# Kernel optimization log

Hardware: AMD Instinct MI355X
Metric: run time of the kernel (lower is better)

## Reference

```python
import jax, jax.numpy as jnp
import numpy as np

H, HKV, HD = 16, 4, 128
EPS = 1.1920928955078125e-07  # float32 eps, torch F.rms_norm default


def _rms_norm(t):
    return t * jax.lax.rsqrt(jnp.mean(t * t, axis=-1, keepdims=True) + EPS)


def _rope(t, cos, sin):
    # t: [B, T, h, HD]; cos/sin: [T, HD//2] -> broadcast [1, T, 1, HD//2]
    te, to = t[..., 0::2], t[..., 1::2]
    c = cos[None, :, None, :]
    s = sin[None, :, None, :]
    re = te * c - to * s
    ro = te * s + to * c
    return jnp.stack((re, ro), axis=-1).reshape(t.shape)


def setup_inputs() -> dict:
    key = jax.random.key(0)
    ks = jax.random.split(key, 5)
    B, T, C = 2, 2048, 2048
    return {
        "x": jax.random.normal(ks[0], (B, T, C), jnp.float32),
        "Wq": jax.random.normal(ks[1], (C, C), jnp.float32) * 0.02,
        "Wk": jax.random.normal(ks[2], (HKV * HD, C), jnp.float32) * 0.02,
        "Wv": jax.random.normal(ks[3], (HKV * HD, C), jnp.float32) * 0.02,
        "Wo": jax.random.normal(ks[4], (C, C), jnp.float32) * 0.02,
        "q_gain": jnp.full((H,), 5.0, jnp.float32),
    }


def reference(x, Wq, Wk, Wv, Wo, q_gain):
    B, T, C = x.shape
    q = (x @ Wq.T).reshape(B, T, H, HD)
    k = (x @ Wk.T).reshape(B, T, HKV, HD)
    v = (x @ Wv.T).reshape(B, T, HKV, HD)

    q = _rms_norm(q)
    k = _rms_norm(k)

    theta = 1.0 / (10000.0 ** (jnp.arange(0, HD, 2, dtype=jnp.float32) / HD))
    t = jnp.arange(T, dtype=jnp.float32)
    freqs = jnp.outer(t, theta)  # [T, HD//2]
    cos, sin = jnp.cos(freqs), jnp.sin(freqs)

    q = _rope(q, cos, sin)
    k = _rope(k, cos, sin)
    q = q * q_gain[None, None, :, None]

    qh = q.transpose(0, 2, 1, 3)                       # [B, H, T, HD]
    kh = jnp.repeat(k.transpose(0, 2, 1, 3), H // HKV, axis=1)
    vh = jnp.repeat(v.transpose(0, 2, 1, 3), H // HKV, axis=1)

    scale = 1.0 / jnp.sqrt(jnp.float32(HD))
    scores = jnp.einsum("bhqd,bhkd->bhqk", qh, kh) * scale
    causal = jnp.tril(jnp.ones((T, T), bool))
    scores = jnp.where(causal[None, None], scores, jnp.finfo(scores.dtype).min)
    attn = jax.nn.softmax(scores, axis=-1)
    out = jnp.einsum("bhqk,bhkd->bhqd", attn, vh)
    out = out.transpose(0, 2, 1, 3).reshape(B, T, C)
    return out @ Wo.T
```

## Files before the change

kernel.cpp:

```cpp
#include <hip/hip_runtime.h>
#include <hip/hip_bf16.h>

#define TSEQ 2048
#define CDIM 2048
#define NH   16
#define NKV  4
#define HDIM 128
#define BATCH 2
#define MROWS (BATCH*TSEQ)
#define KVC   (NKV*HDIM)
#define QKVC  (CDIM + 2*KVC)

typedef short bf16x8 __attribute__((ext_vector_type(8)));
typedef float f32x4  __attribute__((ext_vector_type(4)));

typedef const __attribute__((address_space(1))) void* gptr_t;
typedef __attribute__((address_space(3))) void* sptr_t;

__device__ inline void async16(const __hip_bfloat16* g, __hip_bfloat16* l) {
  __builtin_amdgcn_global_load_lds((gptr_t)g, (sptr_t)l, 16, 0, 0);
}

__device__ inline f32x4 mfma16(bf16x8 a, bf16x8 b, f32x4 c) {
  return __builtin_amdgcn_mfma_f32_16x16x32_bf16(a, b, c, 0, 0, 0);
}

__device__ inline float bfbits2f(unsigned short u) {
  return __uint_as_float(((unsigned)u) << 16);
}

__device__ inline unsigned short f2bfu(float x) {
  __hip_bfloat16 t = __float2bfloat16(x);
  return *(unsigned short*)&t;
}

__device__ inline int swz128(int row, int col) {
  return row*128 + (((col >> 3) ^ (row & 15)) << 3) + (col & 7);
}
__device__ inline int swz64(int row, int col) {
  return row*64 + ((((col >> 3) ^ row) & 7) << 3) + (col & 7);
}

__global__ void canary(const void* __restrict__ x, int* __restrict__ flag) {
  __shared__ int cnt[256];
  int tid = threadIdx.x;
  const unsigned short* u = (const unsigned short*)x;
  int c = 0;
#pragma unroll
  for (int i = 0; i < 4; ++i) {
    float a = fabsf(bfbits2f(u[(tid*4 + i)*2]));
    if (a >= 1e-6f && a <= 1e3f) c++;
  }
  cnt[tid] = c;
  __syncthreads();
  for (int s = 128; s > 0; s >>= 1) {
    if (tid < s) cnt[tid] += cnt[tid + s];
    __syncthreads();
  }
  if (tid == 0) *flag = (cnt[0] > 512) ? 1 : 0;
}

__global__ __launch_bounds__(256) void canonize_all(
    const void* __restrict__ xs,  const void* __restrict__ wqs,
    const void* __restrict__ wks, const void* __restrict__ wvs,
    const void* __restrict__ wos, const void* __restrict__ gs,
    __hip_bfloat16* __restrict__ xd,
    __hip_bfloat16* __restrict__ wqkv,
    __hip_bfloat16* __restrict__ wod,
    __hip_bfloat16* __restrict__ gd,
    const int* __restrict__ flag)
{
  int blk = blockIdx.x;
  const void* src; __hip_bfloat16* dst; int base, n;
  if      (blk < 4096) { src = xs;  dst = xd;                base = blk;        n = MROWS*CDIM; }
  else if (blk < 6144) { src = wqs; dst = wqkv;              base = blk - 4096; n = CDIM*CDIM; }
  else if (blk < 6656) { src = wks; dst = wqkv + (size_t)CDIM*CDIM;            base = blk - 6144; n = KVC*CDIM; }
  else if (blk < 7168) { src = wvs; dst = wqkv + (size_t)(CDIM+KVC)*CDIM;      base = blk - 6656; n = KVC*CDIM; }
  else if (blk < 9216) { src = wos; dst = wod;               base = blk - 7168; n = CDIM*CDIM; }
  else                 { src = gs;  dst = gd;                base = 0;          n = NH; }
  int idx = base*2048 + threadIdx.x*8;
  if (idx >= n) return;
  if (*flag) {
    *(bf16x8*)&dst[idx] = *(const bf16x8*)((const __hip_bfloat16*)src + idx);
  } else {
    const float* s = (const float*)src + idx;
#pragma unroll
    for (int j = 0; j < 8; ++j) dst[idx + j] = __float2bfloat16(s[j]);
  }
}

#define BK 64

__global__ __launch_bounds__(512, 2) void gemm_bt256(
    const __hip_bfloat16* __restrict__ A,
    const __hip_bfloat16* __restrict__ B,
    __hip_bfloat16* __restrict__ C,
    int M, int N, int K, int lda)
{
  __shared__ __align__(16) __hip_bfloat16 As[2][256*BK];
  __shared__ __align__(16) __hip_bfloat16 Bs[2][256*BK];
  const int tid  = threadIdx.x;
  const int wave = tid >> 6;
  const int lane = tid & 63;
  const int qd   = lane >> 4;
  const int ln   = lane & 15;
  const int m0   = blockIdx.y * 256;
  const int n0   = blockIdx.x * 256;
  const int wm   = (wave >> 2) * 128;
  const int wn   = (wave & 3) * 64;

  auto stageA = [&](int half, int buf, int kt) {
    const __hip_bfloat16* src = A + (size_t)(m0 + half*128)*lda + kt*BK;
    __hip_bfloat16* dst = &As[buf][half*128*BK];
#pragma unroll
    for (int i = 0; i < 2; ++i) {
      int c = i*512 + tid;
      int row = c >> 3, sl = c & 7;
      int gs = sl ^ (row & 7);
      async16(&src[(size_t)row*lda + gs*8], &dst[(i*512 + wave*64)*8]);
    }
  };
  auto stageB = [&](int half, int buf, int kt) {
    const __hip_bfloat16* src = B + (size_t)(n0 + half*128)*K + kt*BK;
    __hip_bfloat16* dst = &Bs[buf][half*128*BK];
#pragma unroll
    for (int i = 0; i < 2; ++i) {
      int c = i*512 + tid;
      int row = c >> 3, sl = c & 7;
      int gs = sl ^ (row & 7);
      async16(&src[(size_t)row*K + gs*8], &dst[(i*512 + wave*64)*8]);
    }
  };
  auto ldA = [&](int buf, int m, int kk) -> bf16x8 {
    int row = wm + m*16 + ln;
    return *(const bf16x8*)&As[buf][row*BK + (((kk*4 + qd) ^ (row & 7)) << 3)];
  };
  auto ldB = [&](int buf, int n, int kk) -> bf16x8 {
    int row = wn + n*16 + ln;
    return *(const bf16x8*)&Bs[buf][row*BK + (((kk*4 + qd) ^ (row & 7)) << 3)];
  };

  f32x4 acc[8][4] = {};
  const int nt = K / BK;

  stageA(0, 0, 0); stageA(1, 0, 0);
  stageB(0, 0, 0); stageB(1, 0, 0);
  if (nt > 1) {
    stageA(0, 1, 1); stageA(1, 1, 1);
    asm volatile("s_waitcnt vmcnt(4)" ::: "memory");
  } else {
    asm volatile("s_waitcnt vmcnt(0)" ::: "memory");
  }
  __builtin_amdgcn_s_barrier();

#pragma unroll 1
  for (int t = 0; t < nt; ++t) {
    const int buf = t & 1;
    bf16x8 a03[4][2], a47[4][2], b01[2][2], b23[2][2];

#pragma unroll
    for (int m = 0; m < 4; ++m)
#pragma unroll
      for (int kk = 0; kk < 2; ++kk) a03[m][kk] = ldA(buf, m, kk);
#pragma unroll
    for (int n = 0; n < 2; ++n)
#pragma unroll
      for (int kk = 0; kk < 2; ++kk) b01[n][kk] = ldB(buf, n, kk);
    if (t + 1 < nt) { stageB(0, buf ^ 1, t + 1); stageB(1, buf ^ 1, t + 1); }
    __builtin_amdgcn_s_setprio(1);
#pragma unroll
    for (int m = 0; m < 4; ++m)
#pragma unroll
      for (int n = 0; n < 2; ++n)
#pragma unroll
        for (int kk = 0; kk < 2; ++kk)
          acc[m][n] = mfma16(a03[m][kk], b01[n][kk], acc[m][n]);
    __builtin_amdgcn_s_setprio(0);
    __builtin_amdgcn_s_barrier();

#pragma unroll
    for (int m = 0; m < 4; ++m)
#pragma unroll
      for (int kk = 0; kk < 2; ++kk) a47[m][kk] = ldA(buf, 4 + m, kk);
    __builtin_amdgcn_s_setprio(1);
#pragma unroll
    for (int m = 0; m < 4; ++m)
#pragma unroll
      for (int n = 0; n < 2; ++n)
#pragma unroll
        for (int kk = 0; kk < 2; ++kk)
          acc[4 + m][n] = mfma16(a47[m][kk], b01[n][kk], acc[4 + m][n]);
    __builtin_amdgcn_s_setprio(0);
    __builtin_amdgcn_s_barrier();

#pragma unroll
    for (int n = 0; n < 2; ++n)
#pragma unroll
      for (int kk = 0; kk < 2; ++kk) b23[n][kk] = ldB(buf, 2 + n, kk);
    __builtin_amdgcn_s_setprio(1);
#pragma unroll
    for (int m = 0; m < 4; ++m)
#pragma unroll
      for (int n = 0; n < 2; ++n)
#pragma unroll
        for (int kk = 0; kk < 2; ++kk)
          acc[m][2 + n] = mfma16(a03[m][kk], b23[n][kk], acc[m][2 + n]);
    __builtin_amdgcn_s_setprio(0);
    __builtin_amdgcn_s_barrier();

    if (t + 2 < nt) { stageA(0, buf, t + 2); stageA(1, buf, t + 2); }
    __builtin_amdgcn_s_setprio(1);
#pragma unroll
    for (int m = 0; m < 4; ++m)
#pragma unroll
      for (int n = 0; n < 2; ++n)
#pragma unroll
        for (int kk = 0; kk < 2; ++kk)
          acc[4 + m][2 + n] = mfma16(a47[m][kk], b23[n][kk], acc[4 + m][2 + n]);
    __builtin_amdgcn_s_setprio(0);
    if (t + 2 < nt) asm volatile("s_waitcnt vmcnt(4)" ::: "memory");
    else            asm volatile("s_waitcnt vmcnt(0)" ::: "memory");
    __builtin_amdgcn_s_barrier();
  }

#pragma unroll
  for (int m = 0; m < 8; ++m)
#pragma unroll
    for (int n = 0; n < 4; ++n) {
      int row = m0 + wm + m*16 + qd*4;
      int col = n0 + wn + n*16 + ln;
#pragma unroll
      for (int r = 0; r < 4; ++r)
        C[(size_t)(row + r)*N + col] = __float2bfloat16(acc[m][n][r]);
    }
}

__global__ __launch_bounds__(256, 2) void gemm_out(
    const __hip_bfloat16* __restrict__ A,
    const __hip_bfloat16* __restrict__ B,
    void* __restrict__ C,
    int M, int N, int K, int lda, const int* __restrict__ flag)
{
  __shared__ __align__(16) __hip_bfloat16 As[128*32];
  __shared__ __align__(16) __hip_bfloat16 Bs[128*32];
  const int tid  = threadIdx.x;
  const int wave = tid >> 6;
  const int lane = tid & 63;
  const int qd   = lane >> 4;
  const int ln   = lane & 15;
  const int m0   = blockIdx.y * 128;
  const int n0   = blockIdx.x * 128;
  const int wm   = (wave >> 1) * 64;
  const int wn   = (wave & 1) * 64;

  f32x4 acc[4][4] = {};

  for (int k0 = 0; k0 < K; k0 += 32) {
    __syncthreads();
#pragma unroll
    for (int r = 0; r < 2; ++r) {
      int e   = (r*256 + tid) * 8;
      int row = e >> 5;
      int col = e & 31;
      async16(&A[(size_t)(m0+row)*lda + k0 + col], &As[(size_t)(r*256 + wave*64)*8]);
      async16(&B[(size_t)(n0+row)*K   + k0 + col], &Bs[(size_t)(r*256 + wave*64)*8]);
    }
    __syncthreads();
    bf16x8 af[4], bfr[4];
#pragma unroll
    for (int i = 0; i < 4; ++i)
      af[i] = *(const bf16x8*)&As[(wm + i*16 + ln)*32 + qd*8];
#pragma unroll
    for (int j = 0; j < 4; ++j)
      bfr[j] = *(const bf16x8*)&Bs[(wn + j*16 + ln)*32 + qd*8];
#pragma unroll
    for (int i = 0; i < 4; ++i)
#pragma unroll
      for (int j = 0; j < 4; ++j)
        acc[i][j] = mfma16(af[i], bfr[j], acc[i][j]);
  }
  const bool isbf = (*flag != 0);
#pragma unroll
  for (int i = 0; i < 4; ++i)
#pragma unroll
    for (int j = 0; j < 4; ++j) {
      int row = m0 + wm + i*16 + qd*4;
      int col = n0 + wn + j*16 + ln;
#pragma unroll
      for (int r = 0; r < 4; ++r) {
        if (isbf) ((__hip_bfloat16*)C)[(size_t)(row + r)*N + col] = __float2bfloat16(acc[i][j][r]);
        else      ((float*)C)[(size_t)(row + r)*N + col] = acc[i][j][r];
      }
    }
}

__global__ __launch_bounds__(256) void prep_qk(
    __hip_bfloat16* __restrict__ qkv,
    const __hip_bfloat16* __restrict__ gain)
{
  int wid  = blockIdx.x * 4 + (threadIdx.x >> 6);
  int lane = threadIdx.x & 63;
  bool isq = wid < MROWS*NH;
  int m, h;
  __hip_bfloat16* p;
  if (isq) { m = wid >> 4; h = wid & 15; p = qkv + (size_t)m*QKVC + h*HDIM; }
  else     { int w2 = wid - MROWS*NH; m = w2 >> 2; h = w2 & 3; p = qkv + (size_t)m*QKVC + CDIM + h*HDIM; }

  ushort2 raw = *(const ushort2*)((const unsigned short*)p + 2*lane);
  float e = bfbits2f(raw.x), o = bfbits2f(raw.y);
  float ss = e*e + o*o;
#pragma unroll
  for (int off = 32; off >= 1; off >>= 1) ss += __shfl_xor(ss, off);
  float rms = rsqrtf(ss * (1.0f/128.0f) + 1.1920928955078125e-07f);
  e *= rms; o *= rms;

  float theta = exp2f(-(float)(2*lane) * (1.0f/128.0f) * 13.287712379549449f);
  int t = m & (TSEQ-1);
  float fr = (float)t * theta;
  float c = cosf(fr), s = sinf(fr);
  float re = e*c - o*s;
  float ro = e*s + o*c;

  if (isq) {
    float g = bfbits2f(*(const unsigned short*)&gain[h]) * 0.08838834764831845f;
    re *= g; ro *= g;
  }
  p[2*lane]   = __float2bfloat16(re);
  p[2*lane+1] = __float2bfloat16(ro);
}

__global__ __launch_bounds__(256) void transpose_v(
    const __hip_bfloat16* __restrict__ qkv, __hip_bfloat16* __restrict__ vt)
{
  __shared__ __hip_bfloat16 tile[32][34];
  int tx = threadIdx.x & 31;
  int ty = threadIdx.x >> 5;
  int r0 = blockIdx.x * 32;
  int c0 = blockIdx.y * 32;
#pragma unroll
  for (int i = 0; i < 4; ++i)
    tile[ty + i*8][tx] = qkv[(size_t)(r0 + ty + i*8)*QKVC + (CDIM + KVC) + c0 + tx];
  __syncthreads();
  int b = r0 >> 11;
  int t = r0 & (TSEQ-1);
  int hk = c0 >> 7;
  int d0 = c0 & (HDIM-1);
#pragma unroll
  for (int i = 0; i < 4; ++i) {
    int d = d0 + ty + i*8;
    vt[((size_t)((b*NKV + hk)*HDIM + d))*TSEQ + t + tx] = tile[tx][ty + i*8];
  }
}

__global__ __launch_bounds__(256, 2) void attn_kernel(
    const __hip_bfloat16* __restrict__ qkv,
    const __hip_bfloat16* __restrict__ vt,
    __hip_bfloat16* __restrict__ out)
{
  const int tid  = threadIdx.x;
  const int wave = tid >> 6;
  const int lane = tid & 63;
  const int qd = lane >> 4, ln = lane & 15;
  const int p  = blockIdx.x;
  const int h  = blockIdx.y;
  const int b  = blockIdx.z;
  const int hk = h >> 2;

  const __hip_bfloat16* K = qkv + (size_t)(b*TSEQ)*QKVC + CDIM + hk*HDIM;
  const __hip_bfloat16* V = vt + ((size_t)(b*NKV + hk)*HDIM)*TSEQ;

  __shared__ __align__(16) __hip_bfloat16 Ks[64*128];
  __shared__ __align__(16) __hip_bfloat16 Vs[128*64];
  __shared__ __align__(16) __hip_bfloat16 Pb[64*64];
  __shared__ float Lb[4][64];

  auto issueK = [&](int t0) {
#pragma unroll
    for (int i = 0; i < 4; ++i) {
      int c = i*256 + tid;
      int row = c >> 4, cc = c & 15;
      int gcc = cc ^ (row & 15);
      async16(&K[(size_t)(t0 + row)*QKVC + gcc*8], &Ks[(i*256 + wave*64)*8]);
    }
  };
  auto issueV = [&](int t0) {
#pragma unroll
    for (int i = 0; i < 4; ++i) {
      int c = i*256 + tid;
      int row = c >> 3, cc = c & 7;
      int gcc = cc ^ (row & 7);
      async16(&V[(size_t)row*TSEQ + t0 + gcc*8], &Vs[(i*256 + wave*64)*8]);
    }
  };

#pragma unroll 1
  for (int seg = 0; seg < 2; ++seg) {
    const int qt = seg ? (31 - p) : p;
    const int q0 = qt * 64;

    bf16x8 qfr[4][4];
#pragma unroll
    for (int qsub = 0; qsub < 4; ++qsub)
#pragma unroll
      for (int kc = 0; kc < 4; ++kc)
        qfr[qsub][kc] = *(const bf16x8*)&qkv[((size_t)(b*TSEQ + q0 + qsub*16 + ln))*QKVC + h*HDIM + kc*32 + qd*8];

    f32x4 o[2][4] = {};
    float lacc[4] = {0.f, 0.f, 0.f, 0.f};

    __syncthreads();
    issueK(0);
    __syncthreads();

#pragma unroll 1
    for (int kt = 0; kt <= qt; ++kt) {
      const int t0 = kt * 64;
      issueV(t0);

      f32x4 sc[4] = {};
#pragma unroll
      for (int kc = 0; kc < 4; ++kc) {
        bf16x8 kfa = *(const bf16x8*)&Ks[swz128(wave*16 + ln, kc*32 + qd*8)];
#pragma unroll
        for (int qsub = 0; qsub < 4; ++qsub)
          sc[qsub] = mfma16(kfa, qfr[qsub][kc], sc[qsub]);
      }
      if (kt == qt) {
#pragma unroll
        for (int qsub = 0; qsub < 4; ++qsub)
#pragma unroll
          for (int r = 0; r < 4; ++r) {
            int kv = t0 + wave*16 + qd*4 + r;
            int q  = q0 + qsub*16 + ln;
            if (kv > q) sc[qsub][r] = -1.0e30f;
          }
      }
#pragma unroll
      for (int qsub = 0; qsub < 4; ++qsub) {
#pragma unroll
        for (int r = 0; r < 4; ++r)
          sc[qsub][r] = __expf(sc[qsub][r]);
        lacc[qsub] += (sc[qsub][0] + sc[qsub][1]) + (sc[qsub][2] + sc[qsub][3]);
      }

#pragma unroll
      for (int qsub = 0; qsub < 4; ++qsub) {
        ushort4 pk;
        pk.x = f2bfu(sc[qsub][0]); pk.y = f2bfu(sc[qsub][1]);
        pk.z = f2bfu(sc[qsub][2]); pk.w = f2bfu(sc[qsub][3]);
        *(ushort4*)&Pb[swz64(qsub*16 + ln, wave*16 + qd*4)] = pk;
      }

      __syncthreads();
      if (kt < qt) issueK(t0 + 64);

      __builtin_amdgcn_s_setprio(1);
#pragma unroll
      for (int kc2 = 0; kc2 < 2; ++kc2) {
        bf16x8 pfb[4];
#pragma unroll
        for (int qsub = 0; qsub < 4; ++qsub)
          pfb[qsub] = *(const bf16x8*)&Pb[swz64(qsub*16 + ln, kc2*32 + qd*8)];
#pragma unroll
        for (int half = 0; half < 2; ++half) {
          bf16x8 vfa = *(const bf16x8*)&Vs[swz64(wave*32 + half*16 + ln, kc2*32 + qd*8)];
#pragma unroll
          for (int qsub = 0; qsub < 4; ++qsub)
            o[half][qsub] = mfma16(vfa, pfb[qsub], o[half][qsub]);
        }
      }
      __builtin_amdgcn_s_setprio(0);
      __syncthreads();
    }

#pragma unroll
    for (int qsub = 0; qsub < 4; ++qsub) {
      lacc[qsub] += __shfl_xor(lacc[qsub], 16);
      lacc[qsub] += __shfl_xor(lacc[qsub], 32);
    }
    if (qd == 0) {
#pragma unroll
      for (int qsub = 0; qsub < 4; ++qsub)
        Lb[wave][qsub*16 + ln] = lacc[qsub];
    }
    __syncthreads();
    float inv[4];
#pragma unroll
    for (int qsub = 0; qsub < 4; ++qsub) {
      int q = qsub*16 + ln;
      inv[qsub] = 1.0f / (((Lb[0][q] + Lb[1][q]) + (Lb[2][q] + Lb[3][q])));
    }

#pragma unroll
    for (int half = 0; half < 2; ++half)
#pragma unroll
      for (int qsub = 0; qsub < 4; ++qsub) {
        ushort4 pk;
        pk.x = f2bfu(o[half][qsub][0] * inv[qsub]);
        pk.y = f2bfu(o[half][qsub][1] * inv[qsub]);
        pk.z = f2bfu(o[half][qsub][2] * inv[qsub]);
        pk.w = f2bfu(o[half][qsub][3] * inv[qsub]);
        *(ushort4*)&Ks[swz128(qsub*16 + ln, wave*32 + half*16 + qd*4)] = pk;
      }
    __syncthreads();
#pragma unroll
    for (int pass = 0; pass < 4; ++pass) {
      int row = wave*16 + pass*4 + qd;
      bf16x8 val = *(const bf16x8*)&Ks[swz128(row, ln*8)];
      int q = q0 + row;
      *(bf16x8*)&out[((size_t)(b*TSEQ + q))*CDIM + h*HDIM + ln*8] = val;
    }
  }
}

extern "C" void kernel_launch(void* const* d_in, const int* in_sizes, int n_in,
                              void* d_out, int out_size, void* d_ws, size_t ws_size,
                              hipStream_t stream) {
  char* ws = (char*)d_ws;
  size_t off = 0;
  auto alloc = [&](size_t bytes) { char* p = ws + off; off += (bytes + 255) & ~(size_t)255; return p; };

  int* flag = (int*)alloc(256);
  __hip_bfloat16* xb   = (__hip_bfloat16*)alloc((size_t)MROWS*CDIM*2);
  __hip_bfloat16* wqkv = (__hip_bfloat16*)alloc((size_t)QKVC*CDIM*2);
  __hip_bfloat16* wob  = (__hip_bfloat16*)alloc((size_t)CDIM*CDIM*2);
  __hip_bfloat16* gb   = (__hip_bfloat16*)alloc(256);
  __hip_bfloat16* qkv  = (__hip_bfloat16*)alloc((size_t)MROWS*QKVC*2);
  __hip_bfloat16* vt   = (__hip_bfloat16*)alloc((size_t)MROWS*KVC*2);

  canary<<<1, 256, 0, stream>>>(d_in[0], flag);

  canonize_all<<<9217, 256, 0, stream>>>(
      d_in[0], d_in[1], d_in[2], d_in[3], d_in[4], d_in[5],
      xb, wqkv, wob, gb, flag);

  gemm_bt256<<<dim3(QKVC/256, MROWS/256), 512, 0, stream>>>(
      xb, wqkv, qkv, MROWS, QKVC, CDIM, CDIM);

  int nwaves = MROWS*NH + MROWS*NKV;
  prep_qk<<<nwaves/4, 256, 0, stream>>>(qkv, gb);

  transpose_v<<<dim3(MROWS/32, KVC/32), 256, 0, stream>>>(qkv, vt);

  attn_kernel<<<dim3(16, NH, BATCH), 256, 0, stream>>>(qkv, vt, xb);

  gemm_out<<<dim3(CDIM/128, MROWS/128), 256, 0, stream>>>(
      xb, wob, d_out, MROWS, CDIM, CDIM, CDIM, flag);
}
```

Before: 294.5 us.

## Retile QKV GEMM to 256x192 and rebuild output GEMM with pipelined 128x256 tiles

The QKV projection GEMM moves from 256x256 to 256x192 tiles, so N=3072 splits into 16 column blocks and the grid grows to fill more CUs. The output projection GEMM drops its simple single-buffered 128x128 BK=32 kernel for a 512-thread, double-buffered, swizzled 128x256 BK=64 kernel with async LDS staging and interleaved MFMA phases. Both changes aim to raise MFMA utilisation and hide global-load latency. The cost is more LDS and registers per block, and possibly lower occupancy.

```diff
diff --git a/kernel.cpp b/kernel.cpp
--- a/kernel.cpp
+++ b/kernel.cpp
@@ -98,20 +98,157 @@
     int M, int N, int K, int lda)
 {
   __shared__ __align__(16) __hip_bfloat16 As[2][256*BK];
+  __shared__ __align__(16) __hip_bfloat16 Bs[2][192*BK];
+  const int tid  = threadIdx.x;
+  const int wave = tid >> 6;
+  const int lane = tid & 63;
+  const int qd   = lane >> 4;
+  const int ln   = lane & 15;
+  const int m0   = blockIdx.y * 256;
+  const int n0   = blockIdx.x * 192;
+  const int wm   = (wave >> 2) * 128;
+  const int wn   = (wave & 3) * 48;
+
+  auto stageA = [&](int buf, int kt) {
+    const __hip_bfloat16* src = A + (size_t)m0*lda + kt*BK;
+    __hip_bfloat16* dst = &As[buf][0];
+#pragma unroll
+    for (int i = 0; i < 4; ++i) {
+      int c = i*512 + tid;
+      int row = c >> 3, sl = c & 7;
+      int gs = sl ^ (row & 7);
+      async16(&src[(size_t)row*lda + gs*8], &dst[(i*512 + wave*64)*8]);
+    }
+  };
+  auto stageB = [&](int buf, int kt) {
+    const __hip_bfloat16* src = B + (size_t)n0*K + kt*BK;
+    __hip_bfloat16* dst = &Bs[buf][0];
+#pragma unroll
+    for (int i = 0; i < 3; ++i) {
+      int c = i*512 + tid;
+      int row = c >> 3, sl = c & 7;
+      int gs = sl ^ (row & 7);
+      async16(&src[(size_t)row*K + gs*8], &dst[(i*512 + wave*64)*8]);
+    }
+  };
+  auto ldA = [&](int buf, int m, int kk) -> bf16x8 {
+    int row = wm + m*16 + ln;
+    return *(const bf16x8*)&As[buf][row*BK + (((kk*4 + qd) ^ (row & 7)) << 3)];
+  };
+  auto ldB = [&](int buf, int n, int kk) -> bf16x8 {
+    int row = wn + n*16 + ln;
+    return *(const bf16x8*)&Bs[buf][row*BK + (((kk*4 + qd) ^ (row & 7)) << 3)];
+  };
+
+  f32x4 acc[8][3] = {};
+  const int nt = K / BK;
+
+  stageA(0, 0); stageB(0, 0);
+  if (nt > 1) {
+    stageA(1, 1); stageB(1, 1);
+    asm volatile("s_waitcnt vmcnt(7)" ::: "memory");
+  } else {
+    asm volatile("s_waitcnt vmcnt(0)" ::: "memory");
+  }
+  __builtin_amdgcn_s_barrier();
+
+#pragma unroll 1
+  for (int t = 0; t < nt; ++t) {
+    const int buf = t & 1;
+    bf16x8 a03[4][2], a47[4][2], b01[2][2], b2[2];
+
+#pragma unroll
+    for (int m = 0; m < 4; ++m)
+#pragma unroll
+      for (int kk = 0; kk < 2; ++kk) a03[m][kk] = ldA(buf, m, kk);
+#pragma unroll
+    for (int n = 0; n < 2; ++n)
+#pragma unroll
+      for (int kk = 0; kk < 2; ++kk) b01[n][kk] = ldB(buf, n, kk);
+    __builtin_amdgcn_s_setprio(1);
+#pragma unroll
+    for (int m = 0; m < 4; ++m)
+#pragma unroll
+      for (int n = 0; n < 2; ++n)
+#pragma unroll
+        for (int kk = 0; kk < 2; ++kk)
+          acc[m][n] = mfma16(a03[m][kk], b01[n][kk], acc[m][n]);
+    __builtin_amdgcn_s_setprio(0);
+    __builtin_amdgcn_s_barrier();
+
+#pragma unroll
+    for (int m = 0; m < 4; ++m)
+#pragma unroll
+      for (int kk = 0; kk < 2; ++kk) a47[m][kk] = ldA(buf, 4 + m, kk);
+    __builtin_amdgcn_s_setprio(1);
+#pragma unroll
+    for (int m = 0; m < 4; ++m)
+#pragma unroll
+      for (int n = 0; n < 2; ++n)
+#pragma unroll
+        for (int kk = 0; kk < 2; ++kk)
+          acc[4 + m][n] = mfma16(a47[m][kk], b01[n][kk], acc[4 + m][n]);
+    __builtin_amdgcn_s_setprio(0);
+    __builtin_amdgcn_s_barrier();
+
+#pragma unroll
+    for (int kk = 0; kk < 2; ++kk) b2[kk] = ldB(buf, 2, kk);
+    if (t + 2 < nt) stageA(buf, t + 2);
+    __builtin_amdgcn_s_setprio(1);
+#pragma unroll
+    for (int m = 0; m < 4; ++m)
+#pragma unroll
+      for (int kk = 0; kk < 2; ++kk)
+        acc[m][2] = mfma16(a03[m][kk], b2[kk], acc[m][2]);
+    __builtin_amdgcn_s_setprio(0);
+    __builtin_amdgcn_s_barrier();
+
+    if (t + 2 < nt) stageB(buf, t + 2);
+    __builtin_amdgcn_s_setprio(1);
+#pragma unroll
+    for (int m = 0; m < 4; ++m)
+#pragma unroll
+      for (int kk = 0; kk < 2; ++kk)
+        acc[4 + m][2] = mfma16(a47[m][kk], b2[kk], acc[4 + m][2]);
+    __builtin_amdgcn_s_setprio(0);
+    if (t + 2 < nt) asm volatile("s_waitcnt vmcnt(7)" ::: "memory");
+    else            asm volatile("s_waitcnt vmcnt(0)" ::: "memory");
+    __builtin_amdgcn_s_barrier();
+  }
+
+#pragma unroll
+  for (int m = 0; m < 8; ++m)
+#pragma unroll
+    for (int n = 0; n < 3; ++n) {
+      int row = m0 + wm + m*16 + qd*4;
+      int col = n0 + wn + n*16 + ln;
+#pragma unroll
+      for (int r = 0; r < 4; ++r)
+        C[(size_t)(row + r)*N + col] = __float2bfloat16(acc[m][n][r]);
+    }
+}
+
+__global__ __launch_bounds__(512, 2) void gemm_out(
+    const __hip_bfloat16* __restrict__ A,
+    const __hip_bfloat16* __restrict__ B,
+    void* __restrict__ C,
+    int M, int N, int K, int lda, const int* __restrict__ flag)
+{
+  __shared__ __align__(16) __hip_bfloat16 As[2][128*BK];
   __shared__ __align__(16) __hip_bfloat16 Bs[2][256*BK];
   const int tid  = threadIdx.x;
   const int wave = tid >> 6;
   const int lane = tid & 63;
   const int qd   = lane >> 4;
   const int ln   = lane & 15;
-  const int m0   = blockIdx.y * 256;
+  const int m0   = blockIdx.y * 128;
   const int n0   = blockIdx.x * 256;
-  const int wm   = (wave >> 2) * 128;
+  const int wm   = (wave >> 2) * 64;
   const int wn   = (wave & 3) * 64;
 
-  auto stageA = [&](int half, int buf, int kt) {
-    const __hip_bfloat16* src = A + (size_t)(m0 + half*128)*lda + kt*BK;
-    __hip_bfloat16* dst = &As[buf][half*128*BK];
+  auto stageA = [&](int buf, int kt) {
+    const __hip_bfloat16* src = A + (size_t)m0*lda + kt*BK;
+    __hip_bfloat16* dst = &As[buf][0];
 #pragma unroll
     for (int i = 0; i < 2; ++i) {
       int c = i*512 + tid;
@@ -120,11 +257,11 @@
       async16(&src[(size_t)row*lda + gs*8], &dst[(i*512 + wave*64)*8]);
     }
   };
-  auto stageB = [&](int half, int buf, int kt) {
-    const __hip_bfloat16* src = B + (size_t)(n0 + half*128)*K + kt*BK;
-    __hip_bfloat16* dst = &Bs[buf][half*128*BK];
-#pragma unroll
-    for (int i = 0; i < 2; ++i) {
+  auto stageB = [&](int buf, int kt) {
+    const __hip_bfloat16* src = B + (size_t)n0*K + kt*BK;
+    __hip_bfloat16* dst = &Bs[buf][0];
+#pragma unroll
+    for (int i = 0; i < 4; ++i) {
       int c = i*512 + tid;
       int row = c >> 3, sl = c & 7;
       int gs = sl ^ (row & 7);
@@ -140,14 +277,13 @@
     return *(const bf16x8*)&Bs[buf][row*BK + (((kk*4 + qd) ^ (row & 7)) << 3)];
   };
 
-  f32x4 acc[8][4] = {};
+  f32x4 acc[4][4] = {};
   const int nt = K / BK;
 
-  stageA(0, 0, 0); stageA(1, 0, 0);
-  stageB(0, 0, 0); stageB(1, 0, 0);
+  stageA(0, 0); stageB(0, 0);
   if (nt > 1) {
-    stageA(0, 1, 1); stageA(1, 1, 1);
-    asm volatile("s_waitcnt vmcnt(4)" ::: "memory");
+    stageA(1, 1); stageB(1, 1);
+    asm volatile("s_waitcnt vmcnt(6)" ::: "memory");
   } else {
     asm volatile("s_waitcnt vmcnt(0)" ::: "memory");
   }
@@ -156,40 +292,39 @@
 #pragma unroll 1
   for (int t = 0; t < nt; ++t) {
     const int buf = t & 1;
-    bf16x8 a03[4][2], a47[4][2], b01[2][2], b23[2][2];
-
-#pragma unroll
-    for (int m = 0; m < 4; ++m)
-#pragma unroll
-      for (int kk = 0; kk < 2; ++kk) a03[m][kk] = ldA(buf, m, kk);
+    bf16x8 a01[2][2], a23[2][2], b01[2][2], b23[2][2];
+
+#pragma unroll
+    for (int m = 0; m < 2; ++m)
+#pragma unroll
+      for (int kk = 0; kk < 2; ++kk) a01[m][kk] = ldA(buf, m, kk);
 #pragma unroll
     for (int n = 0; n < 2; ++n)
 #pragma unroll
       for (int kk = 0; kk < 2; ++kk) b01[n][kk] = ldB(buf, n, kk);
-    if (t + 1 < nt) { stageB(0, buf ^ 1, t + 1); stageB(1, buf ^ 1, t + 1); }
-    __builtin_amdgcn_s_setprio(1);
-#pragma unroll
-    for (int m = 0; m < 4; ++m)
+    __builtin_amdgcn_s_setprio(1);
+#pragma unroll
+    for (int m = 0; m < 2; ++m)
 #pragma unroll
       for (int n = 0; n < 2; ++n)
 #pragma unroll
         for (int kk = 0; kk < 2; ++kk)
-          acc[m][n] = mfma16(a03[m][kk], b01[n][kk], acc[m][n]);
-    __builtin_amdgcn_s_setprio(0);
-    __builtin_amdgcn_s_barrier();
-
-#pragma unroll
-    for (int m = 0; m < 4; ++m)
-#pragma unroll
-      for (int kk = 0; kk < 2; ++kk) a47[m][kk] = ldA(buf, 4 + m, kk);
-    __builtin_amdgcn_s_setprio(1);
-#pragma unroll
-    for (int m = 0; m < 4; ++m)
+          acc[m][n] = mfma16(a01[m][kk], b01[n][kk], acc[m][n]);
+    __builtin_amdgcn_s_setprio(0);
+    __builtin_amdgcn_s_barrier();
+
+#pragma unroll
+    for (int m = 0; m < 2; ++m)
+#pragma unroll
+      for (int kk = 0; kk < 2; ++kk) a23[m][kk] = ldA(buf, 2 + m, kk);
+    __builtin_amdgcn_s_setprio(1);
+#pragma unroll
+    for (int m = 0; m < 2; ++m)
 #pragma unroll
       for (int n = 0; n < 2; ++n)
 #pragma unroll
         for (int kk = 0; kk < 2; ++kk)
-          acc[4 + m][n] = mfma16(a47[m][kk], b01[n][kk], acc[4 + m][n]);
+          acc[2 + m][n] = mfma16(a23[m][kk], b01[n][kk], acc[2 + m][n]);
     __builtin_amdgcn_s_setprio(0);
     __builtin_amdgcn_s_barrier();
 
@@ -197,99 +332,44 @@
     for (int n = 0; n < 2; ++n)
 #pragma unroll
       for (int kk = 0; kk < 2; ++kk) b23[n][kk] = ldB(buf, 2 + n, kk);
-    __builtin_amdgcn_s_setprio(1);
-#pragma unroll
-    for (int m = 0; m < 4; ++m)
+    if (t + 2 < nt) stageA(buf, t + 2);
+    __builtin_amdgcn_s_setprio(1);
+#pragma unroll
+    for (int m = 0; m < 2; ++m)
 #pragma unroll
       for (int n = 0; n < 2; ++n)
 #pragma unroll
         for (int kk = 0; kk < 2; ++kk)
-          acc[m][2 + n] = mfma16(a03[m][kk], b23[n][kk], acc[m][2 + n]);
-    __builtin_amdgcn_s_setprio(0);
-    __builtin_amdgcn_s_barrier();
-
-    if (t + 2 < nt) { stageA(0, buf, t + 2); stageA(1, buf, t + 2); }
-    __builtin_amdgcn_s_setprio(1);
-#pragma unroll
-    for (int m = 0; m < 4; ++m)
+          acc[m][2 + n] = mfma16(a01[m][kk], b23[n][kk], acc[m][2 + n]);
+    __builtin_amdgcn_s_setprio(0);
+    __builtin_amdgcn_s_barrier();
+
+    if (t + 2 < nt) stageB(buf, t + 2);
+    __builtin_amdgcn_s_setprio(1);
+#pragma unroll
+    for (int m = 0; m < 2; ++m)
 #pragma unroll
       for (int n = 0; n < 2; ++n)
 #pragma unroll
         for (int kk = 0; kk < 2; ++kk)
-          acc[4 + m][2 + n] = mfma16(a47[m][kk], b23[n][kk], acc[4 + m][2 + n]);
-    __builtin_amdgcn_s_setprio(0);
-    if (t + 2 < nt) asm volatile("s_waitcnt vmcnt(4)" ::: "memory");
+          acc[2 + m][2 + n] = mfma16(a23[m][kk], b23[n][kk], acc[2 + m][2 + n]);
+    __builtin_amdgcn_s_setprio(0);
+    if (t + 2 < nt) asm volatile("s_waitcnt vmcnt(6)" ::: "memory");
     else            asm volatile("s_waitcnt vmcnt(0)" ::: "memory");
     __builtin_amdgcn_s_barrier();
   }
 
-#pragma unroll
-  for (int m = 0; m < 8; ++m)
+  const bool isbf = (*flag != 0);
+#pragma unroll
+  for (int m = 0; m < 4; ++m)
 #pragma unroll
     for (int n = 0; n < 4; ++n) {
       int row = m0 + wm + m*16 + qd*4;
       int col = n0 + wn + n*16 + ln;
 #pragma unroll
-      for (int r = 0; r < 4; ++r)
-        C[(size_t)(row + r)*N + col] = __float2bfloat16(acc[m][n][r]);
-    }
-}
-
-__global__ __launch_bounds__(256, 2) void gemm_out(
-    const __hip_bfloat16* __restrict__ A,
-    const __hip_bfloat16* __restrict__ B,
-    void* __restrict__ C,
-    int M, int N, int K, int lda, const int* __restrict__ flag)
-{
-  __shared__ __align__(16) __hip_bfloat16 As[128*32];
-  __shared__ __align__(16) __hip_bfloat16 Bs[128*32];
-  const int tid  = threadIdx.x;
-  const int wave = tid >> 6;
-  const int lane = tid & 63;
-  const int qd   = lane >> 4;
-  const int ln   = lane & 15;
-  const int m0   = blockIdx.y * 128;
-  const int n0   = blockIdx.x * 128;
-  const int wm   = (wave >> 1) * 64;
-  const int wn   = (wave & 1) * 64;
-
-  f32x4 acc[4][4] = {};
-
-  for (int k0 = 0; k0 < K; k0 += 32) {
-    __syncthreads();
-#pragma unroll
-    for (int r = 0; r < 2; ++r) {
-      int e   = (r*256 + tid) * 8;
-      int row = e >> 5;
-      int col = e & 31;
-      async16(&A[(size_t)(m0+row)*lda + k0 + col], &As[(size_t)(r*256 + wave*64)*8]);
-      async16(&B[(size_t)(n0+row)*K   + k0 + col], &Bs[(size_t)(r*256 + wave*64)*8]);
-    }
-    __syncthreads();
-    bf16x8 af[4], bfr[4];
-#pragma unroll
-    for (int i = 0; i < 4; ++i)
-      af[i] = *(const bf16x8*)&As[(wm + i*16 + ln)*32 + qd*8];
-#pragma unroll
-    for (int j = 0; j < 4; ++j)
-      bfr[j] = *(const bf16x8*)&Bs[(wn + j*16 + ln)*32 + qd*8];
-#pragma unroll
-    for (int i = 0; i < 4; ++i)
-#pragma unroll
-      for (int j = 0; j < 4; ++j)
-        acc[i][j] = mfma16(af[i], bfr[j], acc[i][j]);
-  }
-  const bool isbf = (*flag != 0);
-#pragma unroll
-  for (int i = 0; i < 4; ++i)
-#pragma unroll
-    for (int j = 0; j < 4; ++j) {
-      int row = m0 + wm + i*16 + qd*4;
-      int col = n0 + wn + j*16 + ln;
-#pragma unroll
       for (int r = 0; r < 4; ++r) {
-        if (isbf) ((__hip_bfloat16*)C)[(size_t)(row + r)*N + col] = __float2bfloat16(acc[i][j][r]);
-        else      ((float*)C)[(size_t)(row + r)*N + col] = acc[i][j][r];
+        if (isbf) ((__hip_bfloat16*)C)[(size_t)(row + r)*N + col] = __float2bfloat16(acc[m][n][r]);
+        else      ((float*)C)[(size_t)(row + r)*N + col] = acc[m][n][r];
       }
     }
 }
@@ -534,7 +614,7 @@
       d_in[0], d_in[1], d_in[2], d_in[3], d_in[4], d_in[5],
       xb, wqkv, wob, gb, flag);
 
-  gemm_bt256<<<dim3(QKVC/256, MROWS/256), 512, 0, stream>>>(
+  gemm_bt256<<<dim3(QKVC/192, MROWS/256), 512, 0, stream>>>(
       xb, wqkv, qkv, MROWS, QKVC, CDIM, CDIM);
 
   int nwaves = MROWS*NH + MROWS*NKV;
@@ -544,6 +624,6 @@
 
   attn_kernel<<<dim3(16, NH, BATCH), 256, 0, stream>>>(qkv, vt, xb);
 
-  gemm_out<<<dim3(CDIM/128, MROWS/128), 256, 0, stream>>>(
+  gemm_out<<<dim3(CDIM/256, MROWS/128), 512, 0, stream>>>(
       xb, wob, d_out, MROWS, CDIM, CDIM, CDIM, flag);
 }
```

New measurement: 295.8 us. Within noise of the previous version (+0.5%).

## Retile QKV GEMM to 256x192 tiles, vectorize canonize and prep_qk

Applied to the files above, without the earlier changes.

Changes the fused QKV projection GEMM tile from 256x256 to 256x192. QKVC=3072 then divides into 16 column tiles, for 256 blocks total against the CU count. The staging schedule changes so A and B for tile t+2 are prefetched mid-iteration, with vmcnt thresholds adjusted to match. The fp32->bf16 canonize path now uses float4 loads and a single 16-byte store. prep_qk handles two head-rows per wave with 4-element vector loads and stores. The retiling trades per-block MFMA reuse for better CU balance, and the reordered prefetch schedule risks subtle pipeline hazards.

```diff
diff --git a/kernel.cpp b/kernel.cpp
--- a/kernel.cpp
+++ b/kernel.cpp
@@ -84,8 +84,14 @@
     *(bf16x8*)&dst[idx] = *(const bf16x8*)((const __hip_bfloat16*)src + idx);
   } else {
     const float* s = (const float*)src + idx;
-#pragma unroll
-    for (int j = 0; j < 8; ++j) dst[idx + j] = __float2bfloat16(s[j]);
+    float4 f0 = *(const float4*)s;
+    float4 f1 = *(const float4*)(s + 4);
+    union { bf16x8 v; unsigned short u[8]; } o;
+    o.u[0] = f2bfu(f0.x); o.u[1] = f2bfu(f0.y);
+    o.u[2] = f2bfu(f0.z); o.u[3] = f2bfu(f0.w);
+    o.u[4] = f2bfu(f1.x); o.u[5] = f2bfu(f1.y);
+    o.u[6] = f2bfu(f1.z); o.u[7] = f2bfu(f1.w);
+    *(bf16x8*)&dst[idx] = o.v;
   }
 }
 
@@ -98,33 +104,33 @@
     int M, int N, int K, int lda)
 {
   __shared__ __align__(16) __hip_bfloat16 As[2][256*BK];
-  __shared__ __align__(16) __hip_bfloat16 Bs[2][256*BK];
+  __shared__ __align__(16) __hip_bfloat16 Bs[2][192*BK];
   const int tid  = threadIdx.x;
   const int wave = tid >> 6;
   const int lane = tid & 63;
   const int qd   = lane >> 4;
   const int ln   = lane & 15;
   const int m0   = blockIdx.y * 256;
-  const int n0   = blockIdx.x * 256;
+  const int n0   = blockIdx.x * 192;
   const int wm   = (wave >> 2) * 128;
-  const int wn   = (wave & 3) * 64;
-
-  auto stageA = [&](int half, int buf, int kt) {
-    const __hip_bfloat16* src = A + (size_t)(m0 + half*128)*lda + kt*BK;
-    __hip_bfloat16* dst = &As[buf][half*128*BK];
-#pragma unroll
-    for (int i = 0; i < 2; ++i) {
+  const int wn   = (wave & 3) * 48;
+
+  auto stageA = [&](int buf, int kt) {
+    const __hip_bfloat16* src = A + (size_t)m0*lda + kt*BK;
+    __hip_bfloat16* dst = &As[buf][0];
+#pragma unroll
+    for (int i = 0; i < 4; ++i) {
       int c = i*512 + tid;
       int row = c >> 3, sl = c & 7;
       int gs = sl ^ (row & 7);
       async16(&src[(size_t)row*lda + gs*8], &dst[(i*512 + wave*64)*8]);
     }
   };
-  auto stageB = [&](int half, int buf, int kt) {
-    const __hip_bfloat16* src = B + (size_t)(n0 + half*128)*K + kt*BK;
-    __hip_bfloat16* dst = &Bs[buf][half*128*BK];
-#pragma unroll
-    for (int i = 0; i < 2; ++i) {
+  auto stageB = [&](int buf, int kt) {
+    const __hip_bfloat16* src = B + (size_t)n0*K + kt*BK;
+    __hip_bfloat16* dst = &Bs[buf][0];
+#pragma unroll
+    for (int i = 0; i < 3; ++i) {
       int c = i*512 + tid;
       int row = c >> 3, sl = c & 7;
       int gs = sl ^ (row & 7);
@@ -140,14 +146,13 @@
     return *(const bf16x8*)&Bs[buf][row*BK + (((kk*4 + qd) ^ (row & 7)) << 3)];
   };
 
-  f32x4 acc[8][4] = {};
+  f32x4 acc[8][3] = {};
   const int nt = K / BK;
 
-  stageA(0, 0, 0); stageA(1, 0, 0);
-  stageB(0, 0, 0); stageB(1, 0, 0);
+  stageA(0, 0); stageB(0, 0);
   if (nt > 1) {
-    stageA(0, 1, 1); stageA(1, 1, 1);
-    asm volatile("s_waitcnt vmcnt(4)" ::: "memory");
+    stageA(1, 1); stageB(1, 1);
+    asm volatile("s_waitcnt vmcnt(7)" ::: "memory");
   } else {
     asm volatile("s_waitcnt vmcnt(0)" ::: "memory");
   }
@@ -156,7 +161,7 @@
 #pragma unroll 1
   for (int t = 0; t < nt; ++t) {
     const int buf = t & 1;
-    bf16x8 a03[4][2], a47[4][2], b01[2][2], b23[2][2];
+    bf16x8 a03[4][2], a47[4][2], b01[2][2], b2[2];
 
 #pragma unroll
     for (int m = 0; m < 4; ++m)
@@ -166,7 +171,6 @@
     for (int n = 0; n < 2; ++n)
 #pragma unroll
       for (int kk = 0; kk < 2; ++kk) b01[n][kk] = ldB(buf, n, kk);
-    if (t + 1 < nt) { stageB(0, buf ^ 1, t + 1); stageB(1, buf ^ 1, t + 1); }
     __builtin_amdgcn_s_setprio(1);
 #pragma unroll
     for (int m = 0; m < 4; ++m)
@@ -194,31 +198,26 @@
     __builtin_amdgcn_s_barrier();
 
 #pragma unroll
-    for (int n = 0; n < 2; ++n)
-#pragma unroll
-      for (int kk = 0; kk < 2; ++kk) b23[n][kk] = ldB(buf, 2 + n, kk);
+    for (int kk = 0; kk < 2; ++kk) b2[kk] = ldB(buf, 2, kk);
+    if (t + 2 < nt) stageA(buf, t + 2);
     __builtin_amdgcn_s_setprio(1);
 #pragma unroll
     for (int m = 0; m < 4; ++m)
 #pragma unroll
-      for (int n = 0; n < 2; ++n)
-#pragma unroll
-        for (int kk = 0; kk < 2; ++kk)
-          acc[m][2 + n] = mfma16(a03[m][kk], b23[n][kk], acc[m][2 + n]);
+      for (int kk = 0; kk < 2; ++kk)
+        acc[m][2] = mfma16(a03[m][kk], b2[kk], acc[m][2]);
     __builtin_amdgcn_s_setprio(0);
     __builtin_amdgcn_s_barrier();
 
-    if (t + 2 < nt) { stageA(0, buf, t + 2); stageA(1, buf, t + 2); }
+    if (t + 2 < nt) stageB(buf, t + 2);
     __builtin_amdgcn_s_setprio(1);
 #pragma unroll
     for (int m = 0; m < 4; ++m)
 #pragma unroll
-      for (int n = 0; n < 2; ++n)
-#pragma unroll
-        for (int kk = 0; kk < 2; ++kk)
-          acc[4 + m][2 + n] = mfma16(a47[m][kk], b23[n][kk], acc[4 + m][2 + n]);
+      for (int kk = 0; kk < 2; ++kk)
+        acc[4 + m][2] = mfma16(a47[m][kk], b2[kk], acc[4 + m][2]);
     __builtin_amdgcn_s_setprio(0);
-    if (t + 2 < nt) asm volatile("s_waitcnt vmcnt(4)" ::: "memory");
+    if (t + 2 < nt) asm volatile("s_waitcnt vmcnt(7)" ::: "memory");
     else            asm volatile("s_waitcnt vmcnt(0)" ::: "memory");
     __builtin_amdgcn_s_barrier();
   }
@@ -226,7 +225,7 @@
 #pragma unroll
   for (int m = 0; m < 8; ++m)
 #pragma unroll
-    for (int n = 0; n < 4; ++n) {
+    for (int n = 0; n < 3; ++n) {
       int row = m0 + wm + m*16 + qd*4;
       int col = n0 + wn + n*16 + ln;
 #pragma unroll
@@ -298,35 +297,44 @@
     __hip_bfloat16* __restrict__ qkv,
     const __hip_bfloat16* __restrict__ gain)
 {
-  int wid  = blockIdx.x * 4 + (threadIdx.x >> 6);
+  int wid2 = blockIdx.x * 4 + (threadIdx.x >> 6);
   int lane = threadIdx.x & 63;
-  bool isq = wid < MROWS*NH;
+  int half = lane >> 5;
+  int l32  = lane & 31;
+  int rowid = wid2 * 2 + half;
+  bool isq = rowid < MROWS*NH;
   int m, h;
   __hip_bfloat16* p;
-  if (isq) { m = wid >> 4; h = wid & 15; p = qkv + (size_t)m*QKVC + h*HDIM; }
-  else     { int w2 = wid - MROWS*NH; m = w2 >> 2; h = w2 & 3; p = qkv + (size_t)m*QKVC + CDIM + h*HDIM; }
-
-  ushort2 raw = *(const ushort2*)((const unsigned short*)p + 2*lane);
-  float e = bfbits2f(raw.x), o = bfbits2f(raw.y);
-  float ss = e*e + o*o;
-#pragma unroll
-  for (int off = 32; off >= 1; off >>= 1) ss += __shfl_xor(ss, off);
+  if (isq) { m = rowid >> 4; h = rowid & 15; p = qkv + (size_t)m*QKVC + h*HDIM; }
+  else     { int w2 = rowid - MROWS*NH; m = w2 >> 2; h = w2 & 3; p = qkv + (size_t)m*QKVC + CDIM + h*HDIM; }
+
+  ushort4 raw = *(const ushort4*)((const unsigned short*)p + 4*l32);
+  float e0 = bfbits2f(raw.x), o0 = bfbits2f(raw.y);
+  float e1 = bfbits2f(raw.z), o1 = bfbits2f(raw.w);
+  float ss = (e0*e0 + o0*o0) + (e1*e1 + o1*o1);
+#pragma unroll
+  for (int off = 16; off >= 1; off >>= 1) ss += __shfl_xor(ss, off);
   float rms = rsqrtf(ss * (1.0f/128.0f) + 1.1920928955078125e-07f);
-  e *= rms; o *= rms;
-
-  float theta = exp2f(-(float)(2*lane) * (1.0f/128.0f) * 13.287712379549449f);
+  e0 *= rms; o0 *= rms; e1 *= rms; o1 *= rms;
+
+  int j0 = 2*l32;
+  float th0 = exp2f(-(float)(2*j0)     * (1.0f/128.0f) * 13.287712379549449f);
+  float th1 = exp2f(-(float)(2*j0 + 2) * (1.0f/128.0f) * 13.287712379549449f);
   int t = m & (TSEQ-1);
-  float fr = (float)t * theta;
-  float c = cosf(fr), s = sinf(fr);
-  float re = e*c - o*s;
-  float ro = e*s + o*c;
+  float fr0 = (float)t * th0, fr1 = (float)t * th1;
+  float c0 = cosf(fr0), s0 = sinf(fr0);
+  float c1 = cosf(fr1), s1 = sinf(fr1);
+  float re0 = e0*c0 - o0*s0, ro0 = e0*s0 + o0*c0;
+  float re1 = e1*c1 - o1*s1, ro1 = e1*s1 + o1*c1;
 
   if (isq) {
     float g = bfbits2f(*(const unsigned short*)&gain[h]) * 0.08838834764831845f;
-    re *= g; ro *= g;
-  }
-  p[2*lane]   = __float2bfloat16(re);
-  p[2*lane+1] = __float2bfloat16(ro);
+    re0 *= g; ro0 *= g; re1 *= g; ro1 *= g;
+  }
+  ushort4 outv;
+  outv.x = f2bfu(re0); outv.y = f2bfu(ro0);
+  outv.z = f2bfu(re1); outv.w = f2bfu(ro1);
+  *(ushort4*)((unsigned short*)p + 4*l32) = outv;
 }
 
 __global__ __launch_bounds__(256) void transpose_v(
@@ -534,11 +542,10 @@
       d_in[0], d_in[1], d_in[2], d_in[3], d_in[4], d_in[5],
       xb, wqkv, wob, gb, flag);
 
-  gemm_bt256<<<dim3(QKVC/256, MROWS/256), 512, 0, stream>>>(
+  gemm_bt256<<<dim3(QKVC/192, MROWS/256), 512, 0, stream>>>(
       xb, wqkv, qkv, MROWS, QKVC, CDIM, CDIM);
 
-  int nwaves = MROWS*NH + MROWS*NKV;
-  prep_qk<<<nwaves/4, 256, 0, stream>>>(qkv, gb);
+  prep_qk<<<(MROWS*NH + MROWS*NKV)/8, 256, 0, stream>>>(qkv, gb);
 
   transpose_v<<<dim3(MROWS/32, KVC/32), 256, 0, stream>>>(qkv, vt);
 
```

Measured after the change: 292.8 us. About the same (-0.6%).
